# Kernel optimization log

Hardware: AMD Instinct MI355X
Metric: run time of the kernel (lower is better)

## Reference

```python
import jax, jax.numpy as jnp
import numpy as np
import math

B, T, C = 2, 8192, 1024
H = 16
HD = C // H  # 64
WIN = 256    # local_window_size


def _rope_tables(T, hd):
    inv_freq = 1.0 / (10000.0 ** (np.arange(0, hd, 2, dtype=np.float32) / hd))
    t = np.arange(T, dtype=np.float32)
    freqs = np.outer(t, inv_freq)                      # [T, hd/2]
    emb = np.concatenate([freqs, freqs], axis=-1)      # [T, hd]
    return jnp.asarray(np.cos(emb))[None, None], jnp.asarray(np.sin(emb))[None, None]


def setup_inputs() -> dict:
    key = jax.random.key(0)
    ks = jax.random.split(key, 10)
    x = jax.random.normal(ks[0], (B, T, C), dtype=jnp.float32)
    # padding_mask: bool [B,T]; per the source, True positions end up masked out of attention
    padding_mask = jax.random.randint(ks[1], (B, T), 0, 2).astype(bool)
    cos, sin = _rope_tables(T, HD)                     # [1,1,T,HD]
    s = 1.0 / math.sqrt(C)
    Wq = jax.random.normal(ks[2], (C, C), dtype=jnp.float32) * s
    bq = jnp.zeros((C,), dtype=jnp.float32)
    Wk = jax.random.normal(ks[3], (C, C), dtype=jnp.float32) * s
    bk = jnp.zeros((C,), dtype=jnp.float32)
    Wv = jax.random.normal(ks[4], (C, C), dtype=jnp.float32) * s
    bv = jnp.zeros((C,), dtype=jnp.float32)
    Wo = jax.random.normal(ks[5], (C, C), dtype=jnp.float32) * s
    bo = jnp.zeros((C,), dtype=jnp.float32)
    return {"x": x, "padding_mask": padding_mask, "cos": cos, "sin": sin,
            "Wq": Wq, "bq": bq, "Wk": Wk, "bk": bk, "Wv": Wv, "bv": bv,
            "Wo": Wo, "bo": bo}


def _rotate_half(t):
    h = t.shape[-1] // 2
    return jnp.concatenate([-t[..., h:], t[..., :h]], axis=-1)


def reference(x, padding_mask, cos, sin, Wq, bq, Wk, bk, Wv, bv, Wo, bo):
    Bx, Tx, Cx = x.shape
    Wn = WIN
    pad_end = (Wn - Tx % Wn) % Wn            # static python int
    Tp = Tx + pad_end
    nW = Tp // Wn
    half = Wn // 2
    hd = cos.shape[-1]

    cos_t = jnp.broadcast_to(cos[0, 0][None], (Bx, Tx, hd))
    sin_t = jnp.broadcast_to(sin[0, 0][None], (Bx, Tx, hd))
    if pad_end > 0:
        x = jnp.pad(x, ((0, 0), (0, pad_end), (0, 0)))
        padding_mask = jnp.pad(padding_mask, ((0, 0), (0, pad_end)))
        cos_t = jnp.pad(cos_t, ((0, 0), (0, pad_end), (0, 0)))
        sin_t = jnp.pad(sin_t, ((0, 0), (0, pad_end), (0, 0)))

    # non-overlapping query windows: [B*nW, W, C]
    q_win = x.reshape(Bx * nW, Wn, Cx)
    cos_q = cos_t.reshape(Bx * nW, Wn, hd)[:, None]   # [Bw,1,W,hd]
    sin_q = sin_t.reshape(Bx * nW, Wn, hd)[:, None]

    # overlapping key/value windows of size 2W, stride W
    x_ctx = jnp.pad(x, ((0, 0), (half, half), (0, 0)))
    cos_ctx = jnp.pad(cos_t, ((0, 0), (half, half), (0, 0)))
    sin_ctx = jnp.pad(sin_t, ((0, 0), (half, half), (0, 0)))
    pk = jnp.pad(padding_mask, ((0, 0), (half, half)))  # pad value False
    idx = jnp.arange(nW)[:, None] * Wn + jnp.arange(2 * Wn)[None, :]  # [nW, 2W]
    k_win = x_ctx[:, idx].reshape(Bx * nW, 2 * Wn, Cx)
    cos_k = cos_ctx[:, idx].reshape(Bx * nW, 2 * Wn, hd)[:, None]
    sin_k = sin_ctx[:, idx].reshape(Bx * nW, 2 * Wn, hd)[:, None]
    pk = pk[:, idx].reshape(Bx * nW, 2 * Wn)

    # attn_mask: True = attend (SDPA bool-mask convention)
    attn_mask = ~pk
    all_attend = jnp.all(attn_mask, axis=-1)
    attn_mask = attn_mask.at[:, 0].set(jnp.where(all_attend, False, attn_mask[:, 0]))

    Bw = Bx * nW
    q = (q_win @ Wq.T + bq).reshape(Bw, Wn, H, HD).transpose(0, 2, 1, 3)        # [Bw,H,W,hd]
    k = (k_win @ Wk.T + bk).reshape(Bw, 2 * Wn, H, HD).transpose(0, 2, 1, 3)    # [Bw,H,2W,hd]
    v = (k_win @ Wv.T + bv).reshape(Bw, 2 * Wn, H, HD).transpose(0, 2, 1, 3)

    q = q * cos_q + _rotate_half(q) * sin_q
    k = k * cos_k + _rotate_half(k) * sin_k

    scale = 1.0 / math.sqrt(HD)
    scores = jnp.einsum('bhqd,bhkd->bhqk', q, k) * scale                        # [Bw,H,W,2W]
    scores = jnp.where(attn_mask[:, None, None, :], scores, jnp.finfo(scores.dtype).min)
    attn = jax.nn.softmax(scores, axis=-1)
    out = jnp.einsum('bhqk,bhkd->bhqd', attn, v)
    out = out.transpose(0, 2, 1, 3).reshape(Bw, Wn, Cx)
    out = out @ Wo.T + bo
    out = out.reshape(Bx, nW * Wn, Cx)[:, :Tx]
    return out
```

## Files before the change

### kernel.cpp

```cpp
#include <hip/hip_runtime.h>
#include <hip/hip_bf16.h>
#include <stdint.h>

#define T_SEQ 8192
#define B_SZ 2
#define CDIM 1024
#define NH 16
#define HDIM 64
#define NW 32

typedef unsigned short ushort_t;
typedef __attribute__((ext_vector_type(8))) short short8;
typedef __attribute__((ext_vector_type(8))) unsigned short us8;
typedef __attribute__((ext_vector_type(4))) unsigned short us4;
typedef __attribute__((ext_vector_type(4))) float f32x4;

__device__ __forceinline__ unsigned short f2bf(float f) {
  union { float f; unsigned int u; } c; c.f = f;
  return (unsigned short)((c.u + 0x7FFFu + ((c.u >> 16) & 1u)) >> 16);
}
__device__ __forceinline__ void gld16(void* lds, const void* g) {
  __builtin_amdgcn_global_load_lds(
      (const __attribute__((address_space(1))) void*)g,
      (__attribute__((address_space(3))) void*)lds, 16, 0, 0);
}

__global__ __launch_bounds__(256) void cvt_f32_bf16(const float* __restrict__ src,
                                                    ushort_t* __restrict__ dst, int n4)
{
  int i = blockIdx.x * 256 + threadIdx.x;
  if (i < n4) {
    float4 v = ((const float4*)src)[i];
    ushort4 o;
    o.x = f2bf(v.x); o.y = f2bf(v.y); o.z = f2bf(v.z); o.w = f2bf(v.w);
    ((ushort4*)dst)[i] = o;
  }
}

__global__ __launch_bounds__(256) void cvt_w4(const float* __restrict__ w0,
                                              const float* __restrict__ w1,
                                              const float* __restrict__ w2,
                                              const float* __restrict__ w3,
                                              ushort_t* __restrict__ dst)
{
  const float* srcs[4] = {w0, w1, w2, w3};
  const float* s = srcs[blockIdx.y];
  ushort_t* d = dst + (size_t)blockIdx.y * CDIM * CDIM;
  int i = blockIdx.x * 256 + threadIdx.x;
  float4 v = ((const float4*)s)[i];
  ushort4 o;
  o.x = f2bf(v.x); o.y = f2bf(v.y); o.z = f2bf(v.z); o.w = f2bf(v.w);
  ((ushort4*)d)[i] = o;
}

__device__ __forceinline__ void gemm_core(const ushort_t* __restrict__ A,
                                          const ushort_t* __restrict__ W,
                                          ushort_t* As, ushort_t* Bs,
                                          int m0, int n0, int t, f32x4 acc[4][4])
{
  const int lane = t & 63;
  const int wv = t >> 6;
  const int wm = (wv >> 1) * 64;
  const int wn = (wv & 1) * 64;
  const int fr = lane & 15;
  const int quad = lane >> 4;

  const int srow = t >> 3;
  const int sc8 = ((t & 7) ^ (srow & 7)) * 8;
  const ushort_t* Ag = A + (size_t)(m0 + srow) * CDIM + sc8;
  const ushort_t* Wg = W + (size_t)(n0 + srow) * CDIM + sc8;
  ushort_t* lA = &As[srow * 64 + (t & 7) * 8];
  ushort_t* lB = &Bs[srow * 64 + (t & 7) * 8];

  for (int kt = 0; kt < CDIM; kt += 64) {
    __syncthreads();
#pragma unroll
    for (int p = 0; p < 4; p++) gld16(lA + p * 2048, Ag + (size_t)p * 32 * CDIM + kt);
#pragma unroll
    for (int p = 0; p < 4; p++) gld16(lB + p * 2048, Wg + (size_t)p * 32 * CDIM + kt);
    __syncthreads();
#pragma unroll
    for (int ks = 0; ks < 2; ks++) {
      short8 a[4], b[4];
#pragma unroll
      for (int i = 0; i < 4; i++)
        a[i] = *(const short8*)&As[(wm + i * 16 + fr) * 64 + (((ks * 4 + quad) ^ (fr & 7)) * 8)];
#pragma unroll
      for (int j = 0; j < 4; j++)
        b[j] = *(const short8*)&Bs[(wn + j * 16 + fr) * 64 + (((ks * 4 + quad) ^ (fr & 7)) * 8)];
#pragma unroll
      for (int i = 0; i < 4; i++)
#pragma unroll
        for (int j = 0; j < 4; j++)
          acc[i][j] = __builtin_amdgcn_mfma_f32_16x16x32_bf16(a[i], b[j], acc[i][j], 0, 0, 0);
    }
  }
}

__global__ __launch_bounds__(256, 4) void gemm_qkv(const ushort_t* __restrict__ A,
                                                   const ushort_t* __restrict__ Wcat,
                                                   const float* __restrict__ bq,
                                                   const float* __restrict__ bk,
                                                   const float* __restrict__ bv,
                                                   ushort_t* __restrict__ Qb,
                                                   ushort_t* __restrict__ Kb,
                                                   ushort_t* __restrict__ Vtb,
                                                   const float* __restrict__ cosT,
                                                   const float* __restrict__ sinT)
{
  __shared__ ushort_t SH[17408];
  ushort_t* As = SH;
  ushort_t* Bs = SH + 8192;

  const int t = threadIdx.x;
  const int lane = t & 63;
  const int wv = t >> 6;
  const int wm = (wv >> 1) * 64;
  const int wn = (wv & 1) * 64;
  const int fr = lane & 15;
  const int quad = lane >> 4;
  const int m0 = blockIdx.y * 128;
  const int n0 = blockIdx.x * 128;
  const int sec = blockIdx.x >> 3;
  const int nsec0 = (blockIdx.x & 7) * 128;
  const float* bias = (sec == 0) ? bq : (sec == 1) ? bk : bv;

  f32x4 acc[4][4];
#pragma unroll
  for (int i = 0; i < 4; i++)
#pragma unroll
    for (int j = 0; j < 4; j++) acc[i][j] = (f32x4){0.f, 0.f, 0.f, 0.f};

  gemm_core(A, Wcat, As, Bs, m0, n0, t, acc);

  __syncthreads();

  if (sec < 2) {
    ushort_t* OutQK = sec ? Kb : Qb;
#pragma unroll
    for (int jp = 0; jp < 2; jp++) {
      int d = jp * 16 + fr;
      int cl = wn + jp * 16 + fr;
      float bl = bias[nsec0 + cl];
      float bh = bias[nsec0 + cl + 32];
#pragma unroll
      for (int i = 0; i < 4; i++) {
        int rloc = wm + i * 16 + quad * 4;
#pragma unroll
        for (int r = 0; r < 4; r++) {
          int tt = (m0 + rloc + r) & (T_SEQ - 1);
          float c = cosT[tt * HDIM + d];
          float sn = sinT[tt * HDIM + d];
          float lo = acc[i][jp][r] + bl;
          float hi = acc[i][jp + 2][r] + bh;
          SH[(rloc + r) * 136 + cl] = f2bf(lo * c - hi * sn);
          SH[(rloc + r) * 136 + cl + 32] = f2bf(hi * c + lo * sn);
        }
      }
    }
    __syncthreads();
    const int rr0 = t >> 4;
    const int c8 = (t & 15) * 8;
    size_t gbase = (size_t)m0 * CDIM + nsec0 + c8;
#pragma unroll
    for (int p = 0; p < 8; p++) {
      int rr = p * 16 + rr0;
      *(us8*)&OutQK[gbase + (size_t)rr * CDIM] = *(const us8*)&SH[rr * 136 + c8];
    }
  } else {
#pragma unroll
    for (int j = 0; j < 4; j++) {
      int ch = nsec0 + wn + j * 16 + fr;
      float bvv = bias[ch];
#pragma unroll
      for (int i = 0; i < 4; i++) {
        int m = m0 + wm + i * 16 + quad * 4;
        int bb = m >> 13;
        int tq = m & (T_SEQ - 1);
        us4 pk;
#pragma unroll
        for (int r = 0; r < 4; r++) pk[r] = f2bf(acc[i][j][r] + bvv);
        *(us4*)&Vtb[((size_t)bb * CDIM + ch) * T_SEQ + tq] = pk;
      }
    }
  }
}

__global__ __launch_bounds__(256, 4) void gemm_out(const ushort_t* __restrict__ A,
                                                   const ushort_t* __restrict__ W,
                                                   const float* __restrict__ bias,
                                                   float* __restrict__ Out)
{
  __shared__ ushort_t SH[16384];
  ushort_t* As = SH;
  ushort_t* Bs = SH + 8192;

  const int t = threadIdx.x;
  const int lane = t & 63;
  const int wv = t >> 6;
  const int wm = (wv >> 1) * 64;
  const int wn = (wv & 1) * 64;
  const int fr = lane & 15;
  const int quad = lane >> 4;
  const int m0 = blockIdx.y * 128;
  const int n0 = blockIdx.x * 128;

  f32x4 acc[4][4];
#pragma unroll
  for (int i = 0; i < 4; i++)
#pragma unroll
    for (int j = 0; j < 4; j++) acc[i][j] = (f32x4){0.f, 0.f, 0.f, 0.f};

  gemm_core(A, W, As, Bs, m0, n0, t, acc);

#pragma unroll
  for (int j = 0; j < 4; j++) {
    int n = n0 + wn + j * 16 + fr;
    float bvv = bias[n];
#pragma unroll
    for (int i = 0; i < 4; i++) {
      int m = m0 + wm + i * 16 + quad * 4;
#pragma unroll
      for (int r = 0; r < 4; r++)
        Out[(size_t)(m + r) * CDIM + n] = acc[i][j][r] + bvv;
    }
  }
}

__global__ __launch_bounds__(256) void attn_kernel(const ushort_t* __restrict__ Q,
                                                   const ushort_t* __restrict__ Kg,
                                                   const ushort_t* __restrict__ Vt,
                                                   const int* __restrict__ mask,
                                                   ushort_t* __restrict__ AO)
{
  __shared__ ushort_t Qs[128 * 72];
  __shared__ ushort_t Ks[64 * 72];
  __shared__ ushort_t Vts[64 * 72];
  __shared__ ushort_t Ps[4 * 16 * 72];
  __shared__ unsigned char att[512];

  const int t = threadIdx.x;
  const int lane = t & 63;
  const int wv = t >> 6;
  const int h = blockIdx.x;
  const int w = blockIdx.y >> 1;
  const int qh = blockIdx.y & 1;
  const int b = blockIdx.z;

  bool a0, a1;
  {
    int p0 = w * 256 + t - 128;
    a0 = (p0 < 0 || p0 >= T_SEQ) ? true : (mask[b * T_SEQ + p0] == 0);
    int p1 = p0 + 256;
    a1 = (p1 < 0 || p1 >= T_SEQ) ? true : (mask[b * T_SEQ + p1] == 0);
  }
  int all1 = __syncthreads_and((int)(a0 && a1));
  att[t] = a0 ? 1 : 0;
  att[t + 256] = a1 ? 1 : 0;
  if (all1 && t == 0) att[0] = 0;

  {
    int row = t >> 3;
    int c8 = (t & 7) * 8;
    size_t qbase = ((size_t)b * T_SEQ + w * 256 + qh * 128) * CDIM + h * HDIM + c8;
#pragma unroll
    for (int p = 0; p < 4; p++) {
      int r = p * 32 + row;
      *(us8*)&Qs[r * 72 + c8] = *(const us8*)&Q[qbase + (size_t)r * CDIM];
    }
  }

  const int fr = lane & 15;
  const int quad = lane >> 4;
  const int kq = quad * 8;
  const ushort_t* vt_base = Vt + ((size_t)b * CDIM + h * HDIM) * T_SEQ;
  const float SCL = 0.18033688011112042f;

  float m_run[2][4], l_run[2][4];
  f32x4 o[2][4];
#pragma unroll
  for (int mt = 0; mt < 2; mt++)
#pragma unroll
    for (int r = 0; r < 4; r++) { m_run[mt][r] = -3.0e38f; l_run[mt][r] = 0.f; }
#pragma unroll
  for (int mt = 0; mt < 2; mt++)
#pragma unroll
    for (int nt = 0; nt < 4; nt++) o[mt][nt] = (f32x4){0.f, 0.f, 0.f, 0.f};

  for (int kc = 0; kc < 8; kc++) {
    __syncthreads();
    {
      int row = t >> 3;
      int c8 = (t & 7) * 8;
#pragma unroll
      for (int p = 0; p < 2; p++) {
        int jj = p * 32 + row;
        int pos = w * 256 + kc * 64 + jj - 128;
        us8 kval = (us8)(0);
        if (pos >= 0 && pos < T_SEQ)
          kval = *(const us8*)&Kg[((size_t)b * T_SEQ + pos) * CDIM + h * HDIM + c8];
        *(us8*)&Ks[jj * 72 + c8] = kval;
      }
    }
    {
      int dd = t >> 3;
      int kg = (t & 7) * 8;
      int pos0 = w * 256 + kc * 64 - 128 + kg;
      bool inr = (pos0 >= 0) && (pos0 < T_SEQ);
#pragma unroll
      for (int p = 0; p < 2; p++) {
        int d = p * 32 + dd;
        us8 vv = (us8)(0);
        if (inr) vv = *(const us8*)&vt_base[(size_t)d * T_SEQ + pos0];
        *(us8*)&Vts[d * 72 + kg] = vv;
      }
    }
    __syncthreads();

    short8 afr[2][2], bfr[4][2];
#pragma unroll
    for (int mt = 0; mt < 2; mt++)
#pragma unroll
      for (int ks = 0; ks < 2; ks++)
        afr[mt][ks] = *(const short8*)&Qs[(wv * 32 + mt * 16 + fr) * 72 + ks * 32 + kq];
#pragma unroll
    for (int nt = 0; nt < 4; nt++)
#pragma unroll
      for (int ks = 0; ks < 2; ks++)
        bfr[nt][ks] = *(const short8*)&Ks[(nt * 16 + fr) * 72 + ks * 32 + kq];

    f32x4 s[2][4];
#pragma unroll
    for (int mt = 0; mt < 2; mt++)
#pragma unroll
      for (int nt = 0; nt < 4; nt++) {
        f32x4 a = (f32x4){0.f, 0.f, 0.f, 0.f};
        a = __builtin_amdgcn_mfma_f32_16x16x32_bf16(afr[mt][0], bfr[nt][0], a, 0, 0, 0);
        a = __builtin_amdgcn_mfma_f32_16x16x32_bf16(afr[mt][1], bfr[nt][1], a, 0, 0, 0);
        s[mt][nt] = a;
      }

    float kb[4];
#pragma unroll
    for (int nt = 0; nt < 4; nt++)
      kb[nt] = att[kc * 64 + nt * 16 + fr] ? 0.f : -1.0e38f;
#pragma unroll
    for (int mt = 0; mt < 2; mt++)
#pragma unroll
      for (int nt = 0; nt < 4; nt++)
#pragma unroll
        for (int r = 0; r < 4; r++)
          s[mt][nt][r] = __builtin_fmaf(s[mt][nt][r], SCL, kb[nt]);

#pragma unroll
    for (int mt = 0; mt < 2; mt++) {
#pragma unroll
      for (int r = 0; r < 4; r++) {
        float mm = fmaxf(fmaxf(s[mt][0][r], s[mt][1][r]), fmaxf(s[mt][2][r], s[mt][3][r]));
        for (int off = 1; off < 16; off <<= 1) mm = fmaxf(mm, __shfl_xor(mm, off, 64));
        float mnew = fmaxf(m_run[mt][r], mm);
        float alpha = __builtin_amdgcn_exp2f(m_run[mt][r] - mnew);
        float rs = 0.f;
#pragma unroll
        for (int nt = 0; nt < 4; nt++) {
          float p = __builtin_amdgcn_exp2f(s[mt][nt][r] - mnew);
          s[mt][nt][r] = p;
          rs += p;
        }
        for (int off = 1; off < 16; off <<= 1) rs += __shfl_xor(rs, off, 64);
        l_run[mt][r] = l_run[mt][r] * alpha + rs;
        m_run[mt][r] = mnew;
#pragma unroll
        for (int nt = 0; nt < 4; nt++) o[mt][nt][r] *= alpha;
      }
    }

    short8 vf[4][2];
#pragma unroll
    for (int nt = 0; nt < 4; nt++)
#pragma unroll
      for (int ks = 0; ks < 2; ks++)
        vf[nt][ks] = *(const short8*)&Vts[(nt * 16 + fr) * 72 + ks * 32 + kq];

    ushort_t* pw = &Ps[wv * 16 * 72];
    const int rot_r = 8 * (fr >> 2);
#pragma unroll
    for (int mt = 0; mt < 2; mt++) {
#pragma unroll
      for (int nt = 0; nt < 4; nt++) {
#pragma unroll
        for (int r = 0; r < 4; r++) {
          int cs = ((nt * 16 + fr) + 8 * quad) & 63;
          pw[(quad * 4 + r) * 72 + cs] = f2bf(s[mt][nt][r]);
        }
      }
      short8 pf[2];
#pragma unroll
      for (int ks = 0; ks < 2; ks++)
        pf[ks] = *(const short8*)&pw[fr * 72 + ((ks * 32 + kq + rot_r) & 63)];
#pragma unroll
      for (int nt = 0; nt < 4; nt++) {
        o[mt][nt] = __builtin_amdgcn_mfma_f32_16x16x32_bf16(pf[0], vf[nt][0], o[mt][nt], 0, 0, 0);
        o[mt][nt] = __builtin_amdgcn_mfma_f32_16x16x32_bf16(pf[1], vf[nt][1], o[mt][nt], 0, 0, 0);
      }
    }
  }

  size_t obase = ((size_t)b * T_SEQ + w * 256 + qh * 128) * CDIM + h * HDIM;
#pragma unroll
  for (int mt = 0; mt < 2; mt++)
#pragma unroll
    for (int r = 0; r < 4; r++) {
      int row = wv * 32 + mt * 16 + quad * 4 + r;
      float inv = 1.0f / fmaxf(l_run[mt][r], 1e-30f);
#pragma unroll
      for (int nt = 0; nt < 4; nt++) {
        int col = nt * 16 + fr;
        AO[obase + (size_t)row * CDIM + col] = f2bf(o[mt][nt][r] * inv);
      }
    }
}

extern "C" void kernel_launch(void* const* d_in, const int* in_sizes, int n_in,
                              void* d_out, int out_size, void* d_ws, size_t ws_size,
                              hipStream_t stream)
{
  const float* x    = (const float*)d_in[0];
  const int*   pm   = (const int*)d_in[1];
  const float* cosT = (const float*)d_in[2];
  const float* sinT = (const float*)d_in[3];
  const float* Wq   = (const float*)d_in[4];
  const float* bq   = (const float*)d_in[5];
  const float* Wk   = (const float*)d_in[6];
  const float* bk   = (const float*)d_in[7];
  const float* Wv   = (const float*)d_in[8];
  const float* bv   = (const float*)d_in[9];
  const float* Wo   = (const float*)d_in[10];
  const float* bo   = (const float*)d_in[11];
  float* out = (float*)d_out;

  const size_t NTOK = (size_t)B_SZ * T_SEQ;
  const size_t NELT = NTOK * CDIM;
  ushort_t* Kb  = (ushort_t*)d_out;
  ushort_t* xbf = (ushort_t*)d_out + NELT;
  char* ws = (char*)d_ws;
  ushort_t* Wbf = (ushort_t*)ws;
  ushort_t* Qb  = (ushort_t*)(ws + 4 * (size_t)CDIM * CDIM * 2);
  ushort_t* Vtb = Qb + NELT;
  ushort_t* AO  = Qb;

  cvt_f32_bf16<<<(int)(NELT / 4 / 256), 256, 0, stream>>>(x, xbf, (int)(NELT / 4));
  cvt_w4<<<dim3(CDIM * CDIM / 4 / 256, 4), 256, 0, stream>>>(Wq, Wk, Wv, Wo, Wbf);

  gemm_qkv<<<dim3(24, (int)(NTOK / 128)), 256, 0, stream>>>(
      xbf, Wbf, bq, bk, bv, Qb, Kb, Vtb, cosT, sinT);

  attn_kernel<<<dim3(NH, NW * 2, B_SZ), 256, 0, stream>>>(Qb, Kb, Vtb, pm, AO);

  gemm_out<<<dim3(8, (int)(NTOK / 128)), 256, 0, stream>>>(
      AO, Wbf + 3 * (size_t)CDIM * CDIM, bo, out);
}
```

Baseline: 437.5 us.

## Restructure attention inner loop with transposed S, lazy rescale, packed bf16 P

The attention kernel now keeps Q fragments in registers instead of LDS and computes S transposed (K as the A operand), so each lane owns one query row and row reductions need only two cross-lane shuffles. Rescaling of the running max is skipped unless the new max exceeds the old one by more than a threshold, and P is written to LDS as packed bf16 pairs via v_cvt_pk_bf16_f32 with an XOR swizzle. The mask is stored as float biases read as vectors, and launch bounds ask for 4 blocks per CU. This is meant to cut LDS traffic, shuffle and exp work and to raise occupancy, at the cost of more per-row broadcasts of alpha and l and some numeric headroom from lazy rescaling.

```diff
diff --git a/kernel.cpp b/kernel.cpp
--- a/kernel.cpp
+++ b/kernel.cpp
@@ -18,6 +18,11 @@
 __device__ __forceinline__ unsigned short f2bf(float f) {
   union { float f; unsigned int u; } c; c.f = f;
   return (unsigned short)((c.u + 0x7FFFu + ((c.u >> 16) & 1u)) >> 16);
+}
+__device__ __forceinline__ unsigned pk2(float a, float b) {
+  unsigned r;
+  asm("v_cvt_pk_bf16_f32 %0, %1, %2" : "=v"(r) : "v"(a), "v"(b));
+  return r;
 }
 __device__ __forceinline__ void gld16(void* lds, const void* g) {
   __builtin_amdgcn_global_load_lds(
@@ -227,17 +232,16 @@
   }
 }
 
-__global__ __launch_bounds__(256) void attn_kernel(const ushort_t* __restrict__ Q,
-                                                   const ushort_t* __restrict__ Kg,
-                                                   const ushort_t* __restrict__ Vt,
-                                                   const int* __restrict__ mask,
-                                                   ushort_t* __restrict__ AO)
-{
-  __shared__ ushort_t Qs[128 * 72];
+__global__ __launch_bounds__(256, 4) void attn_kernel(const ushort_t* __restrict__ Q,
+                                                      const ushort_t* __restrict__ Kg,
+                                                      const ushort_t* __restrict__ Vt,
+                                                      const int* __restrict__ mask,
+                                                      ushort_t* __restrict__ AO)
+{
   __shared__ ushort_t Ks[64 * 72];
   __shared__ ushort_t Vts[64 * 72];
-  __shared__ ushort_t Ps[4 * 16 * 72];
-  __shared__ unsigned char att[512];
+  __shared__ unsigned int PsW[4 * 32 * 32];
+  __shared__ float attf[512];
 
   const int t = threadIdx.x;
   const int lane = t & 63;
@@ -246,42 +250,45 @@
   const int w = blockIdx.y >> 1;
   const int qh = blockIdx.y & 1;
   const int b = blockIdx.z;
-
-  bool a0, a1;
+  const int fr = lane & 15;
+  const int quad = lane >> 4;
+
   {
     int p0 = w * 256 + t - 128;
-    a0 = (p0 < 0 || p0 >= T_SEQ) ? true : (mask[b * T_SEQ + p0] == 0);
+    bool a0 = (p0 < 0 || p0 >= T_SEQ) ? true : (mask[b * T_SEQ + p0] == 0);
     int p1 = p0 + 256;
-    a1 = (p1 < 0 || p1 >= T_SEQ) ? true : (mask[b * T_SEQ + p1] == 0);
-  }
-  int all1 = __syncthreads_and((int)(a0 && a1));
-  att[t] = a0 ? 1 : 0;
-  att[t + 256] = a1 ? 1 : 0;
-  if (all1 && t == 0) att[0] = 0;
-
+    bool a1 = (p1 < 0 || p1 >= T_SEQ) ? true : (mask[b * T_SEQ + p1] == 0);
+    int all1 = __syncthreads_and((int)(a0 && a1));
+    attf[t] = a0 ? 0.f : -1.0e38f;
+    attf[t + 256] = a1 ? 0.f : -1.0e38f;
+    if (all1 && t == 0) attf[0] = -1.0e38f;
+  }
+
+  short8 qf[2][2];
   {
-    int row = t >> 3;
-    int c8 = (t & 7) * 8;
-    size_t qbase = ((size_t)b * T_SEQ + w * 256 + qh * 128) * CDIM + h * HDIM + c8;
-#pragma unroll
-    for (int p = 0; p < 4; p++) {
-      int r = p * 32 + row;
-      *(us8*)&Qs[r * 72 + c8] = *(const us8*)&Q[qbase + (size_t)r * CDIM];
-    }
-  }
-
-  const int fr = lane & 15;
-  const int quad = lane >> 4;
-  const int kq = quad * 8;
+    const ushort_t* qp = Q + ((size_t)b * T_SEQ + w * 256 + qh * 128 + wv * 32 + fr) * CDIM
+                           + h * HDIM + quad * 8;
+#pragma unroll
+    for (int mt = 0; mt < 2; mt++)
+#pragma unroll
+      for (int ks = 0; ks < 2; ks++)
+        qf[mt][ks] = *(const short8*)&qp[(size_t)mt * 16 * CDIM + ks * 32];
+  }
+
+  const int srow = t >> 3;
+  const int sc8 = (t & 7) * 8;
+  const ushort_t* kgb = Kg + (size_t)b * T_SEQ * CDIM + h * HDIM + sc8;
   const ushort_t* vt_base = Vt + ((size_t)b * CDIM + h * HDIM) * T_SEQ;
   const float SCL = 0.18033688011112042f;
 
-  float m_run[2][4], l_run[2][4];
+  unsigned int* pw = &PsW[wv * 1024];
+  const int swz = (fr & 7) << 2;
+  const int rbase = quad << 2;
+
+  float m_run[2], l_run[2];
   f32x4 o[2][4];
 #pragma unroll
-  for (int mt = 0; mt < 2; mt++)
-#pragma unroll
-    for (int r = 0; r < 4; r++) { m_run[mt][r] = -3.0e38f; l_run[mt][r] = 0.f; }
+  for (int mt = 0; mt < 2; mt++) { m_run[mt] = -3.0e38f; l_run[mt] = 0.f; }
 #pragma unroll
   for (int mt = 0; mt < 2; mt++)
 #pragma unroll
@@ -290,89 +297,98 @@
   for (int kc = 0; kc < 8; kc++) {
     __syncthreads();
     {
-      int row = t >> 3;
-      int c8 = (t & 7) * 8;
 #pragma unroll
       for (int p = 0; p < 2; p++) {
-        int jj = p * 32 + row;
+        int jj = p * 32 + srow;
         int pos = w * 256 + kc * 64 + jj - 128;
         us8 kval = (us8)(0);
-        if (pos >= 0 && pos < T_SEQ)
-          kval = *(const us8*)&Kg[((size_t)b * T_SEQ + pos) * CDIM + h * HDIM + c8];
-        *(us8*)&Ks[jj * 72 + c8] = kval;
-      }
-    }
-    {
-      int dd = t >> 3;
-      int kg = (t & 7) * 8;
-      int pos0 = w * 256 + kc * 64 - 128 + kg;
+        if (pos >= 0 && pos < T_SEQ) kval = *(const us8*)&kgb[(size_t)pos * CDIM];
+        *(us8*)&Ks[jj * 72 + sc8] = kval;
+      }
+      int pos0 = w * 256 + kc * 64 - 128 + sc8;
       bool inr = (pos0 >= 0) && (pos0 < T_SEQ);
 #pragma unroll
       for (int p = 0; p < 2; p++) {
-        int d = p * 32 + dd;
+        int d = p * 32 + srow;
         us8 vv = (us8)(0);
         if (inr) vv = *(const us8*)&vt_base[(size_t)d * T_SEQ + pos0];
-        *(us8*)&Vts[d * 72 + kg] = vv;
+        *(us8*)&Vts[d * 72 + sc8] = vv;
       }
     }
     __syncthreads();
 
-    short8 afr[2][2], bfr[4][2];
-#pragma unroll
-    for (int mt = 0; mt < 2; mt++)
+    short8 kf[4][2];
+#pragma unroll
+    for (int nt = 0; nt < 4; nt++)
 #pragma unroll
       for (int ks = 0; ks < 2; ks++)
-        afr[mt][ks] = *(const short8*)&Qs[(wv * 32 + mt * 16 + fr) * 72 + ks * 32 + kq];
-#pragma unroll
-    for (int nt = 0; nt < 4; nt++)
-#pragma unroll
-      for (int ks = 0; ks < 2; ks++)
-        bfr[nt][ks] = *(const short8*)&Ks[(nt * 16 + fr) * 72 + ks * 32 + kq];
-
-    f32x4 s[2][4];
+        kf[nt][ks] = *(const short8*)&Ks[(nt * 16 + fr) * 72 + ks * 32 + quad * 8];
+
+    f32x4 st[2][4];
 #pragma unroll
     for (int mt = 0; mt < 2; mt++)
 #pragma unroll
       for (int nt = 0; nt < 4; nt++) {
         f32x4 a = (f32x4){0.f, 0.f, 0.f, 0.f};
-        a = __builtin_amdgcn_mfma_f32_16x16x32_bf16(afr[mt][0], bfr[nt][0], a, 0, 0, 0);
-        a = __builtin_amdgcn_mfma_f32_16x16x32_bf16(afr[mt][1], bfr[nt][1], a, 0, 0, 0);
-        s[mt][nt] = a;
-      }
-
-    float kb[4];
+        a = __builtin_amdgcn_mfma_f32_16x16x32_bf16(kf[nt][0], qf[mt][0], a, 0, 0, 0);
+        a = __builtin_amdgcn_mfma_f32_16x16x32_bf16(kf[nt][1], qf[mt][1], a, 0, 0, 0);
+        st[mt][nt] = a;
+      }
+
+    f32x4 kb[4];
 #pragma unroll
     for (int nt = 0; nt < 4; nt++)
-      kb[nt] = att[kc * 64 + nt * 16 + fr] ? 0.f : -1.0e38f;
+      kb[nt] = *(const f32x4*)&attf[kc * 64 + nt * 16 + quad * 4];
 #pragma unroll
     for (int mt = 0; mt < 2; mt++)
 #pragma unroll
       for (int nt = 0; nt < 4; nt++)
 #pragma unroll
         for (int r = 0; r < 4; r++)
-          s[mt][nt][r] = __builtin_fmaf(s[mt][nt][r], SCL, kb[nt]);
+          st[mt][nt][r] = __builtin_fmaf(st[mt][nt][r], SCL, kb[nt][r]);
 
 #pragma unroll
     for (int mt = 0; mt < 2; mt++) {
-#pragma unroll
-      for (int r = 0; r < 4; r++) {
-        float mm = fmaxf(fmaxf(s[mt][0][r], s[mt][1][r]), fmaxf(s[mt][2][r], s[mt][3][r]));
-        for (int off = 1; off < 16; off <<= 1) mm = fmaxf(mm, __shfl_xor(mm, off, 64));
-        float mnew = fmaxf(m_run[mt][r], mm);
-        float alpha = __builtin_amdgcn_exp2f(m_run[mt][r] - mnew);
-        float rs = 0.f;
-#pragma unroll
-        for (int nt = 0; nt < 4; nt++) {
-          float p = __builtin_amdgcn_exp2f(s[mt][nt][r] - mnew);
-          s[mt][nt][r] = p;
+      float t0 = fmaxf(fmaxf(st[mt][0][0], st[mt][0][1]), fmaxf(st[mt][0][2], st[mt][0][3]));
+      float t1 = fmaxf(fmaxf(st[mt][1][0], st[mt][1][1]), fmaxf(st[mt][1][2], st[mt][1][3]));
+      float t2 = fmaxf(fmaxf(st[mt][2][0], st[mt][2][1]), fmaxf(st[mt][2][2], st[mt][2][3]));
+      float t3 = fmaxf(fmaxf(st[mt][3][0], st[mt][3][1]), fmaxf(st[mt][3][2], st[mt][3][3]));
+      float mx = fmaxf(fmaxf(t0, t1), fmaxf(t2, t3));
+      mx = fmaxf(mx, __shfl_xor(mx, 16, 64));
+      mx = fmaxf(mx, __shfl_xor(mx, 32, 64));
+      if (!__all(mx <= m_run[mt] + 8.f)) {
+        float mnew = fmaxf(m_run[mt], mx);
+        float alpha = __builtin_amdgcn_exp2f(m_run[mt] - mnew);
+        m_run[mt] = mnew;
+        l_run[mt] *= alpha;
+        float af[4];
+#pragma unroll
+        for (int r = 0; r < 4; r++) af[r] = __shfl(alpha, rbase + r, 64);
+#pragma unroll
+        for (int nt = 0; nt < 4; nt++)
+#pragma unroll
+          for (int r = 0; r < 4; r++) o[mt][nt][r] *= af[r];
+      }
+      float rs = 0.f;
+#pragma unroll
+      for (int nt = 0; nt < 4; nt++)
+#pragma unroll
+        for (int r = 0; r < 4; r++) {
+          float p = __builtin_amdgcn_exp2f(st[mt][nt][r] - m_run[mt]);
+          st[mt][nt][r] = p;
           rs += p;
         }
-        for (int off = 1; off < 16; off <<= 1) rs += __shfl_xor(rs, off, 64);
-        l_run[mt][r] = l_run[mt][r] * alpha + rs;
-        m_run[mt][r] = mnew;
-#pragma unroll
-        for (int nt = 0; nt < 4; nt++) o[mt][nt][r] *= alpha;
-      }
+      rs += __shfl_xor(rs, 16, 64);
+      rs += __shfl_xor(rs, 32, 64);
+      l_run[mt] += rs;
+
+      unsigned int* pr = pw + ((mt * 16 + fr) << 5);
+#pragma unroll
+      for (int nt = 0; nt < 4; nt++)
+#pragma unroll
+        for (int hh = 0; hh < 2; hh++)
+          pr[(((nt << 3) + (quad << 1) + hh)) ^ swz] =
+              pk2(st[mt][nt][2 * hh], st[mt][nt][2 * hh + 1]);
     }
 
     short8 vf[4][2];
@@ -380,24 +396,15 @@
     for (int nt = 0; nt < 4; nt++)
 #pragma unroll
       for (int ks = 0; ks < 2; ks++)
-        vf[nt][ks] = *(const short8*)&Vts[(nt * 16 + fr) * 72 + ks * 32 + kq];
-
-    ushort_t* pw = &Ps[wv * 16 * 72];
-    const int rot_r = 8 * (fr >> 2);
+        vf[nt][ks] = *(const short8*)&Vts[(nt * 16 + fr) * 72 + ks * 32 + quad * 8];
+
 #pragma unroll
     for (int mt = 0; mt < 2; mt++) {
-#pragma unroll
-      for (int nt = 0; nt < 4; nt++) {
-#pragma unroll
-        for (int r = 0; r < 4; r++) {
-          int cs = ((nt * 16 + fr) + 8 * quad) & 63;
-          pw[(quad * 4 + r) * 72 + cs] = f2bf(s[mt][nt][r]);
-        }
-      }
+      const unsigned int* pr = pw + ((mt * 16 + fr) << 5);
       short8 pf[2];
 #pragma unroll
       for (int ks = 0; ks < 2; ks++)
-        pf[ks] = *(const short8*)&pw[fr * 72 + ((ks * 32 + kq + rot_r) & 63)];
+        pf[ks] = *(const short8*)&pr[((ks << 4) + (quad << 2)) ^ swz];
 #pragma unroll
       for (int nt = 0; nt < 4; nt++) {
         o[mt][nt] = __builtin_amdgcn_mfma_f32_16x16x32_bf16(pf[0], vf[nt][0], o[mt][nt], 0, 0, 0);
@@ -406,18 +413,17 @@
     }
   }
 
-  size_t obase = ((size_t)b * T_SEQ + w * 256 + qh * 128) * CDIM + h * HDIM;
+  size_t obase = ((size_t)b * T_SEQ + w * 256 + qh * 128 + wv * 32) * CDIM + h * HDIM;
 #pragma unroll
   for (int mt = 0; mt < 2; mt++)
 #pragma unroll
     for (int r = 0; r < 4; r++) {
-      int row = wv * 32 + mt * 16 + quad * 4 + r;
-      float inv = 1.0f / fmaxf(l_run[mt][r], 1e-30f);
-#pragma unroll
-      for (int nt = 0; nt < 4; nt++) {
-        int col = nt * 16 + fr;
-        AO[obase + (size_t)row * CDIM + col] = f2bf(o[mt][nt][r] * inv);
-      }
+      float lv = __shfl(l_run[mt], rbase + r, 64);
+      float iv = 1.0f / fmaxf(lv, 1e-30f);
+      int row = mt * 16 + quad * 4 + r;
+#pragma unroll
+      for (int nt = 0; nt < 4; nt++)
+        AO[obase + (size_t)row * CDIM + nt * 16 + fr] = f2bf(o[mt][nt][r] * iv);
     }
 }
 
```

New measurement: 420.8 us. -3.8%, faster.
